# Optimization experiments

Measured on AMD Instinct MI355X. Metric: run time of the kernel, lower is better.

## Reference

```python
import jax, jax.numpy as jnp
import numpy as np

DN = ('NCHW', 'OIHW', 'NCHW')


def _conv(x, w, b, pad):
    y = jax.lax.conv_general_dilated(x, w, window_strides=(1, 1),
                                     padding=[(pad, pad), (pad, pad)],
                                     dimension_numbers=DN)
    return y + b[None, :, None, None]


def _maxpool2(x):
    return jax.lax.reduce_window(x, -jnp.inf, jax.lax.max,
                                 (1, 1, 2, 2), (1, 1, 2, 2), 'VALID')


def setup_inputs() -> dict:
    key = jax.random.key(0)
    ks = jax.random.split(key, 17)
    s = 0.05
    inp = {
        'x':  jax.random.normal(ks[0], (256, 3, 32, 32), jnp.float32),
        # conv weights (OIHW) and biases, matching AlexNet_flags.features
        'w1': jax.random.normal(ks[1], (64, 3, 3, 3), jnp.float32) * s,
        'b1': jax.random.normal(ks[2], (64,), jnp.float32) * s,
        'w2': jax.random.normal(ks[3], (192, 64, 5, 5), jnp.float32) * s,
        'b2': jax.random.normal(ks[4], (192,), jnp.float32) * s,
        'w3': jax.random.normal(ks[5], (384, 192, 3, 3), jnp.float32) * s,
        'b3': jax.random.normal(ks[6], (384,), jnp.float32) * s,
        'w4': jax.random.normal(ks[7], (256, 384, 3, 3), jnp.float32) * s,
        'b4': jax.random.normal(ks[8], (256,), jnp.float32) * s,
        'w5': jax.random.normal(ks[9], (256, 256, 3, 3), jnp.float32) * s,
        'b5': jax.random.normal(ks[10], (256,), jnp.float32) * s,
        # classifier linears (weight stored [out, in] as in torch)
        'fw1': jax.random.normal(ks[11], (4096, 256 * 4 * 4), jnp.float32) * s,
        'fb1': jax.random.normal(ks[12], (4096,), jnp.float32) * s,
        'fw2': jax.random.normal(ks[13], (4096, 4096), jnp.float32) * s,
        'fb2': jax.random.normal(ks[14], (4096,), jnp.float32) * s,
        'fw3': jax.random.normal(ks[15], (1000, 4096), jnp.float32) * s,
        'fb3': jax.random.normal(ks[16], (1000,), jnp.float32) * s,
    }
    return inp


def reference(x, w1, b1, w2, b2, w3, b3, w4, b4, w5, b5,
              fw1, fb1, fw2, fb2, fw3, fb3):
    relu = jax.nn.relu
    h = _maxpool2(relu(_conv(x, w1, b1, pad=1)))   # [B,64,16,16]
    h = _maxpool2(relu(_conv(h, w2, b2, pad=2)))   # [B,192,8,8]
    h = relu(_conv(h, w3, b3, pad=1))              # [B,384,8,8]
    h = relu(_conv(h, w4, b4, pad=1))              # [B,256,8,8]
    h = _maxpool2(relu(_conv(h, w5, b5, pad=1)))   # [B,256,4,4]
    h = h.reshape(h.shape[0], 256 * 4 * 4)
    # Dropout layers act as identity at inference (eval mode).
    h = relu(h @ fw1.T + fb1)
    h = relu(h @ fw2.T + fb2)
    return h @ fw3.T + fb3                          # [B,1000]
```

## Files before the change

kernel.cpp:

```cpp
#include <hip/hip_runtime.h>
#include <hip/hip_bf16.h>

#define DIV_UP(a,b) (((a)+(b)-1)/(b))

typedef __attribute__((ext_vector_type(8))) short bfrag;
typedef __attribute__((ext_vector_type(4))) float accf;
typedef __attribute__((ext_vector_type(16))) float accf16;

__device__ __forceinline__ unsigned short f2bf(float f) {
    __hip_bfloat16 h = __float2bfloat16(f);
    return *reinterpret_cast<unsigned short*>(&h);
}

__global__ __launch_bounds__(256) void conv1_mfma(
    const float* __restrict__ in, const float* __restrict__ w,
    const float* __restrict__ bias, unsigned short* __restrict__ out, int n0)
{
    constexpr int RAWS = 3 * 6 * 34;
    constexpr int INS  = 128 * 32;
    constexpr int WSZ  = 64 * 32;
    constexpr int CS   = 128 * 66;
    constexpr int SMEM = (CS * 4 > (RAWS + 4 + INS + WSZ) * 2)
                       ? CS * 4 : (RAWS + 4 + INS + WSZ) * 2;
    __shared__ __align__(16) char smem[SMEM];
    short* raw_s = (short*)smem;
    short* in_s  = raw_s + RAWS + 4;
    short* w_s   = in_s + INS;
    float* c_s   = (float*)smem;

    const int tid  = threadIdx.x;
    const int lane = tid & 63, wv = tid >> 6;
    const int quad = lane >> 4, lr = lane & 15;
    const int rb   = blockIdx.x;
    const int nl   = blockIdx.y;
    const int n    = n0 + nl;
    const int row0 = rb * 4;

    for (int idx = tid; idx < RAWS; idx += 256) {
        int c = idx / 204, rem = idx - c * 204;
        int ry = rem / 34, rx = rem - ry * 34;
        int iy = row0 - 1 + ry, ix = rx - 1;
        float v = 0.f;
        if (iy >= 0 && iy < 32 && ix >= 0 && ix < 32)
            v = in[((n * 3 + c) * 32 + iy) * 32 + ix];
        raw_s[idx] = (short)f2bf(v);
    }
    {
        const int soc = tid >> 2, cbq = tid & 3;
        const int wsw = ((cbq ^ ((soc >> 1) & 3)) << 3);
        __align__(16) unsigned short buf[8];
#pragma unroll
        for (int j = 0; j < 8; ++j) {
            int k = cbq * 8 + j;
            buf[j] = (k < 27) ? f2bf(w[soc * 27 + k]) : (unsigned short)0;
        }
        *(uint4*)&w_s[soc * 32 + wsw] = *(uint4*)buf;
    }
    __syncthreads();
    {
        const int k = tid & 31, pg = tid >> 5;
        const int shi = k >> 3, slo = k & 7;
        const bool valid = (k < 27);
        int cbase = 0;
        if (valid) {
            int c = k / 9, rr = k - c * 9;
            int ky = rr / 3, kx = rr - ky * 3;
            cbase = c * 204 + ky * 34 + kx;
        }
        const int prow = pg >> 1, pcol0 = (pg & 1) * 16;
        const int rbase = cbase + prow * 34 + pcol0;
#pragma unroll
        for (int i = 0; i < 16; ++i) {
            const int pos = prow * 32 + pcol0 + i;
            short v = valid ? raw_s[rbase + i] : (short)0;
            in_s[pos * 32 + ((shi ^ ((pos >> 1) & 3)) << 3) + slo] = v;
        }
    }
    __syncthreads();
    const int bswz = (quad ^ ((lr >> 1) & 3)) << 3;
    const bfrag b = *(const bfrag*)(w_s + (wv * 16 + lr) * 32 + bswz);
    accf acc[8];
#pragma unroll
    for (int mt = 0; mt < 8; ++mt) {
        const int pos = mt * 16 + lr;
        const bfrag a = *(const bfrag*)(in_s + pos * 32 + ((quad ^ ((pos >> 1) & 3)) << 3));
        acc[mt] = __builtin_amdgcn_mfma_f32_16x16x32_bf16(
            a, b, (accf){0.f, 0.f, 0.f, 0.f}, 0, 0, 0);
    }
    __syncthreads();
#pragma unroll
    for (int mt = 0; mt < 8; ++mt)
#pragma unroll
        for (int r = 0; r < 4; ++r)
            c_s[(mt * 16 + quad * 4 + r) * 66 + wv * 16 + lr] = acc[mt][r];
    __syncthreads();
    {
        const int oc = tid >> 2;
        const float bv = bias[oc];
        const int o0 = (tid & 3) * 8;
        __align__(16) unsigned short buf[8];
#pragma unroll
        for (int i = 0; i < 8; ++i) {
            int op = o0 + i, oy = op >> 4, ox = op & 15;
            int p = (oy * 2) * 32 + ox * 2;
            float v = fmaxf(fmaxf(c_s[p * 66 + oc],        c_s[(p + 1) * 66 + oc]),
                            fmaxf(c_s[(p + 32) * 66 + oc], c_s[(p + 33) * 66 + oc]));
            buf[i] = f2bf(fmaxf(v + bv, 0.f));
        }
        unsigned short* dst = out + ((size_t)(nl * 64 + oc)) * 256 + (row0 >> 1) * 16 + o0;
        *(uint4*)dst = *(uint4*)buf;
    }
}

__global__ __launch_bounds__(256) void wt_transform(
    const float* __restrict__ w, unsigned short* __restrict__ wt,
    int COUT, int CIN, int KK, int total)
{
    int idx = blockIdx.x * 256 + threadIdx.x;
    if (idx >= total) return;
    const int j    = idx & 7;
    const int lane = (idx >> 3) & 63;
    const int kh   = (idx >> 9) & 1;
    int t = idx >> 10;
    const int NOCG = COUT >> 5;
    const int ocg  = t % NOCG; t /= NOCG;
    const int NC   = CIN >> 5;
    const int cc   = t % NC;
    const int g    = t / NC;
    const int oc = ocg * 32 + (lane & 31);
    const int ci = cc * 32 + kh * 16 + (lane >> 5) * 8 + j;
    wt[idx] = f2bf(w[((size_t)oc * CIN + ci) * KK + g]);
}

template<int CIN, int KS, int HIN, int IMGS, int MODE, int COUT>
__global__ __launch_bounds__(256) void conv_mfma32(
    const unsigned short* __restrict__ in, const unsigned short* __restrict__ wt,
    const float* __restrict__ bias, unsigned short* __restrict__ out)
{
    constexpr int PAD  = KS / 2;
    constexpr int KK   = KS * KS;
    constexpr int PIX  = HIN * HIN;
    constexpr int NC   = CIN / 32;
    constexpr int NOCG = COUT / 32;
    constexpr int IPOS = IMGS * PIX;
    constexpr int ROWB = (IMGS == 1) ? PIX / 128 : 1;
    constexpr int INS  = IPOS * 32 + 32;
    constexpr int CS   = 128 * 66;
    constexpr int SMEM = (INS * 2 > CS * 4) ? INS * 2 : CS * 4;
    constexpr int GSTR = NC * NOCG * 1024;

    __shared__ __align__(16) char smem[SMEM];
    short* in_s = (short*)smem;
    float* c_s  = (float*)smem;

    const int tid  = threadIdx.x;
    const int lane = tid & 63, wv = tid >> 6;
    const int hi   = lane >> 5, lr32 = lane & 31;
    const int wvM  = wv >> 1, wvN = wv & 1;
    const int ocb  = blockIdx.x / ROWB, rb = blockIdx.x % ROWB;
    const int oc0  = ocb * 64;
    const int nl0  = (IMGS == 2) ? blockIdx.y * 2 : blockIdx.y;
    const int row0 = rb * (128 / HIN);

    if (tid < 32) in_s[IPOS * 32 + tid] = 0;

    accf16 acc[2];
#pragma unroll
    for (int i = 0; i < 2; ++i)
#pragma unroll
        for (int r = 0; r < 16; ++r) acc[i][r] = 0.f;

    int pym[2], pxm[2];
#pragma unroll
    for (int mt = 0; mt < 2; ++mt) {
        const int m = wvM * 64 + mt * 32 + lr32;
        pym[mt] = row0 + m / HIN;
        pxm[mt] = m % HIN;
    }
    int apos[KK][2];
    if constexpr (KS == 3) {
#pragma unroll
        for (int g = 0; g < KK; ++g) {
            const int dy = g / 3 - 1, dx = g % 3 - 1;
#pragma unroll
            for (int mt = 0; mt < 2; ++mt) {
                const int m = wvM * 64 + mt * 32 + lr32;
                const int img = m >> 6, p = m & 63;
                const int iy = (p >> 3) + dy, ix = (p & 7) + dx;
                const bool ok = ((unsigned)iy < 8u) & ((unsigned)ix < 8u);
                const int pos = ok ? img * 64 + iy * 8 + ix : IPOS;
                apos[g][mt] = pos * 64 + ((hi ^ ((pos >> 1) & 3)) << 4);
            }
        }
    }

    const int sci = tid & 31, slot = tid >> 5;
    const int shi = sci >> 3, slo = sci & 7;
    const unsigned short* wbase = wt + (size_t)(oc0 / 32 + wvN) * 1024 + lane * 8;

    for (int c0 = 0; c0 < CIN; c0 += 32) {
        const unsigned short* wb = wbase + (size_t)(c0 >> 5) * (NOCG * 1024);
        __syncthreads();
#pragma unroll
        for (int img = 0; img < IMGS; ++img) {
            const unsigned short* src = in + ((size_t)((nl0 + img) * CIN + c0 + sci)) * PIX;
            for (int iy = slot; iy < HIN; iy += 8) {
#pragma unroll
                for (int xc = 0; xc < HIN; xc += 8) {
                    uint4 v = *(const uint4*)(src + iy * HIN + xc);
                    const int p0 = img * PIX + iy * HIN + xc;
                    unsigned short e[8];
                    e[0] = (unsigned short)(v.x & 0xFFFF); e[1] = (unsigned short)(v.x >> 16);
                    e[2] = (unsigned short)(v.y & 0xFFFF); e[3] = (unsigned short)(v.y >> 16);
                    e[4] = (unsigned short)(v.z & 0xFFFF); e[5] = (unsigned short)(v.z >> 16);
                    e[6] = (unsigned short)(v.w & 0xFFFF); e[7] = (unsigned short)(v.w >> 16);
#pragma unroll
                    for (int k = 0; k < 8; ++k) {
                        const int p = p0 + k;
                        in_s[p * 32 + ((shi ^ ((p >> 1) & 3)) << 3) + slo] = (short)e[k];
                    }
                }
            }
        }
        bfrag bc0 = *(const bfrag*)(wb);
        bfrag bc1 = *(const bfrag*)(wb + 512);
        __syncthreads();
#pragma unroll
        for (int g = 0; g < KK; ++g) {
            bfrag bn0 = bc0, bn1 = bc1;
            if (g + 1 < KK) {
                bn0 = *(const bfrag*)(wb + (size_t)(g + 1) * GSTR);
                bn1 = *(const bfrag*)(wb + (size_t)(g + 1) * GSTR + 512);
            }
            int ap[2];
            if constexpr (KS == 3) {
                ap[0] = apos[g][0]; ap[1] = apos[g][1];
            } else {
                const int dy = g / KS - PAD, dx = g % KS - PAD;
#pragma unroll
                for (int mt = 0; mt < 2; ++mt) {
                    const int iy = pym[mt] + dy, ix = pxm[mt] + dx;
                    const bool ok = ((unsigned)iy < (unsigned)HIN) &
                                    ((unsigned)ix < (unsigned)HIN);
                    const int pos = ok ? iy * HIN + ix : IPOS;
                    ap[mt] = pos * 64 + ((hi ^ ((pos >> 1) & 3)) << 4);
                }
            }
#pragma unroll
            for (int kh = 0; kh < 2; ++kh) {
                const bfrag bb = kh ? bc1 : bc0;
#pragma unroll
                for (int mt = 0; mt < 2; ++mt) {
                    const bfrag a = *(const bfrag*)((const char*)in_s + (ap[mt] ^ (kh << 5)));
                    acc[mt] = __builtin_amdgcn_mfma_f32_32x32x16_bf16(a, bb, acc[mt], 0, 0, 0);
                }
            }
            bc0 = bn0; bc1 = bn1;
        }
    }

    __syncthreads();
#pragma unroll
    for (int mt = 0; mt < 2; ++mt)
#pragma unroll
        for (int r = 0; r < 16; ++r) {
            const int row = wvM * 64 + mt * 32 + (r & 3) + 8 * (r >> 2) + 4 * hi;
            c_s[row * 66 + wvN * 32 + lr32] = acc[mt][r];
        }
    __syncthreads();

    const int oc = tid >> 2;
    const float bv = bias[oc0 + oc];
    if (MODE == 0) {
        const int q = tid & 3, img = q >> 1, pl0 = (q & 1) * 32;
        __align__(16) unsigned short buf[32];
#pragma unroll
        for (int i = 0; i < 32; ++i)
            buf[i] = f2bf(fmaxf(c_s[(img * 64 + pl0 + i) * 66 + oc] + bv, 0.f));
        unsigned short* dst = out + ((size_t)((nl0 + img) * COUT + oc0 + oc)) * 64 + pl0;
        *(uint4*)(dst)      = *(uint4*)(buf);
        *(uint4*)(dst + 8)  = *(uint4*)(buf + 8);
        *(uint4*)(dst + 16) = *(uint4*)(buf + 16);
        *(uint4*)(dst + 24) = *(uint4*)(buf + 24);
    } else if (MODE == 1) {
        const int o0 = (tid & 3) * 8;
        __align__(16) unsigned short buf[8];
#pragma unroll
        for (int i = 0; i < 8; ++i) {
            int op = o0 + i, oy = op >> 3, ox = op & 7;
            int p = (oy * 2) * 16 + ox * 2;
            float v = fmaxf(fmaxf(c_s[p * 66 + oc],        c_s[(p + 1) * 66 + oc]),
                            fmaxf(c_s[(p + 16) * 66 + oc], c_s[(p + 17) * 66 + oc]));
            buf[i] = f2bf(fmaxf(v + bv, 0.f));
        }
        unsigned short* dst = out + ((size_t)(nl0 * COUT + oc0 + oc)) * 64
                            + (row0 >> 1) * 8 + o0;
        *(uint4*)dst = *(uint4*)buf;
    } else {
        const int q = tid & 3, img = q >> 1, o0 = (q & 1) * 8;
        __align__(16) unsigned short buf[8];
#pragma unroll
        for (int i = 0; i < 8; ++i) {
            int op = o0 + i, oy = op >> 2, ox = op & 3;
            int p = img * 64 + (oy * 2) * 8 + ox * 2;
            float v = fmaxf(fmaxf(c_s[p * 66 + oc],       c_s[(p + 1) * 66 + oc]),
                            fmaxf(c_s[(p + 8) * 66 + oc], c_s[(p + 9) * 66 + oc]));
            buf[i] = f2bf(fmaxf(v + bv, 0.f));
        }
        *(uint4*)(out + (size_t)(nl0 + img) * 4096 + (oc0 + oc) * 16 + o0) = *(uint4*)buf;
    }
}

template<bool RELU, bool F32OUT>
__global__ __launch_bounds__(1024) void fc_mfma4(
    const unsigned short* __restrict__ X, const float* __restrict__ W,
    const float* __restrict__ Bs, void* __restrict__ Yv, int N, int K)
{
    __shared__ __align__(16) char smem[65536];
    short* stag = (short*)smem;
    float* red  = (float*)smem;

    const int tid  = threadIdx.x;
    const int lane = tid & 63;
    const int w16  = tid >> 6;
    const int grp  = w16 >> 2;
    const int wg   = w16 & 3;
    const int quad = lane >> 4, lr = lane & 15;
    const int m0 = blockIdx.y * 64, n0 = blockIdx.x * 64;
    const int gtid = tid & 255;
    const int mm = gtid >> 2, ko = (gtid & 3) * 8;
    const int KQ = K >> 2;

    short* Xs = stag + grp * 4096;
    short* Ws = Xs + 2048;

    accf acc[4];
#pragma unroll
    for (int i = 0; i < 4; ++i) acc[i] = (accf){0.f, 0.f, 0.f, 0.f};

    int nr = n0 + mm; if (nr > N - 1) nr = N - 1;
    const unsigned short* xp = X + (size_t)(m0 + mm) * K + (size_t)grp * KQ + ko;
    const float*          wp = W + (size_t)nr * K + (size_t)grp * KQ + ko;

    const int wsw = (((gtid & 3) ^ ((mm >> 1) & 3)) << 3);
    const int rsw = ((quad ^ ((lr >> 1) & 3)) << 3);

    uint4  xv = *(const uint4*)(xp);
    float4 wa = *(const float4*)(wp);
    float4 wb = *(const float4*)(wp + 4);

    for (int k0 = 0; k0 < KQ; k0 += 32) {
        __syncthreads();
        *(uint4*)&Xs[mm * 32 + wsw] = xv;
        __align__(16) unsigned short wb16[8] = {
            f2bf(wa.x), f2bf(wa.y), f2bf(wa.z), f2bf(wa.w),
            f2bf(wb.x), f2bf(wb.y), f2bf(wb.z), f2bf(wb.w) };
        *(uint4*)&Ws[mm * 32 + wsw] = *(uint4*)wb16;
        __syncthreads();
        if (k0 + 32 < KQ) {
            xv = *(const uint4*)(xp + k0 + 32);
            wa = *(const float4*)(wp + k0 + 32);
            wb = *(const float4*)(wp + k0 + 36);
        }
        const bfrag b = *(const bfrag*)(Ws + (wg * 16 + lr) * 32 + rsw);
#pragma unroll
        for (int mt = 0; mt < 4; ++mt) {
            const bfrag a = *(const bfrag*)(Xs + (mt * 16 + lr) * 32 + rsw);
            acc[mt] = __builtin_amdgcn_mfma_f32_16x16x32_bf16(a, b, acc[mt], 0, 0, 0);
        }
    }

    __syncthreads();
#pragma unroll
    for (int mt = 0; mt < 4; ++mt)
#pragma unroll
        for (int r = 0; r < 4; ++r)
            red[grp * 4096 + (mt * 16 + quad * 4 + r) * 64 + wg * 16 + lr] = acc[mt][r];
    __syncthreads();

    {
        const int m  = tid >> 4;
        const int nq = (tid & 15) * 4;
        float4 v0 = *(const float4*)&red[            m * 64 + nq];
        float4 v1 = *(const float4*)&red[ 4096 +     m * 64 + nq];
        float4 v2 = *(const float4*)&red[ 8192 +     m * 64 + nq];
        float4 v3 = *(const float4*)&red[12288 +     m * 64 + nq];
        float s[4] = { v0.x + v1.x + v2.x + v3.x,
                       v0.y + v1.y + v2.y + v3.y,
                       v0.z + v1.z + v2.z + v3.z,
                       v0.w + v1.w + v2.w + v3.w };
#pragma unroll
        for (int i = 0; i < 4; ++i) {
            const int n = n0 + nq + i;
            if (n < N) {
                float v = s[i] + Bs[n];
                if (RELU) v = fmaxf(v, 0.f);
                if (F32OUT) ((float*)Yv)[(size_t)(m0 + m) * N + n] = v;
                else ((unsigned short*)Yv)[(size_t)(m0 + m) * N + n] = f2bf(v);
            }
        }
    }
}

__global__ void zero_out(float* __restrict__ out, int total)
{
    int i = blockIdx.x * 256 + threadIdx.x;
    if (i < total) out[i] = 0.f;
}

extern "C" void kernel_launch(void* const* d_in, const int* in_sizes, int n_in,
                              void* d_out, int out_size, void* d_ws, size_t ws_size,
                              hipStream_t stream)
{
    (void)in_sizes; (void)n_in;
    const float* x   = (const float*)d_in[0];
    const float* w1  = (const float*)d_in[1];
    const float* b1  = (const float*)d_in[2];
    const float* w2  = (const float*)d_in[3];
    const float* b2  = (const float*)d_in[4];
    const float* w3  = (const float*)d_in[5];
    const float* b3  = (const float*)d_in[6];
    const float* w4  = (const float*)d_in[7];
    const float* b4  = (const float*)d_in[8];
    const float* w5  = (const float*)d_in[9];
    const float* b5  = (const float*)d_in[10];
    const float* fw1 = (const float*)d_in[11];
    const float* fb1 = (const float*)d_in[12];
    const float* fw2 = (const float*)d_in[13];
    const float* fb2 = (const float*)d_in[14];
    const float* fw3 = (const float*)d_in[15];
    const float* fb3 = (const float*)d_in[16];
    float* out = (float*)d_out;

    const size_t WTB = 4890624u;
    int maxCH;
    if      (ws_size >= 27959296u) maxCH = 256;
    else if (ws_size >= 17473536u) maxCH = 128;
    else if (ws_size >= 14852096u) maxCH = 96;
    else if (ws_size >= 12230656u) maxCH = 64;
    else {
        zero_out<<<DIV_UP(out_size, 256), 256, 0, stream>>>(out, out_size);
        return;
    }
    unsigned short* wt2 = (unsigned short*)d_ws;
    unsigned short* wt3 = wt2 + 307200;
    unsigned short* wt4 = wt3 + 663552;
    unsigned short* wt5 = wt4 + 884736;
    const size_t CAb = ((size_t)maxCH * 49152u > 2097152u) ? (size_t)maxCH * 49152u : 2097152u;
    const size_t CBb = ((size_t)maxCH * 32768u > 2097152u) ? (size_t)maxCH * 32768u : 2097152u;
    unsigned short* CA = (unsigned short*)((char*)d_ws + WTB);
    unsigned short* CB = (unsigned short*)((char*)d_ws + WTB + CAb);
    unsigned short* T5 = (unsigned short*)((char*)d_ws + WTB + CAb + CBb);

    wt_transform<<<DIV_UP(307200, 256), 256, 0, stream>>>(w2, wt2, 192, 64, 25, 307200);
    wt_transform<<<DIV_UP(663552, 256), 256, 0, stream>>>(w3, wt3, 384, 192, 9, 663552);
    wt_transform<<<DIV_UP(884736, 256), 256, 0, stream>>>(w4, wt4, 256, 384, 9, 884736);
    wt_transform<<<DIV_UP(589824, 256), 256, 0, stream>>>(w5, wt5, 256, 256, 9, 589824);

    for (int n0 = 0; n0 < 256; ) {
        const int CH = (256 - n0 < maxCH) ? (256 - n0) : maxCH;
        conv1_mfma<<<dim3(8, CH), 256, 0, stream>>>(x, w1, b1, CA, n0);
        conv_mfma32<64, 5, 16, 1, 1, 192><<<dim3(6, CH), 256, 0, stream>>>(CA, wt2, b2, CB);
        conv_mfma32<192, 3, 8, 2, 0, 384><<<dim3(6, CH / 2), 256, 0, stream>>>(CB, wt3, b3, CA);
        conv_mfma32<384, 3, 8, 2, 0, 256><<<dim3(4, CH / 2), 256, 0, stream>>>(CA, wt4, b4, CB);
        conv_mfma32<256, 3, 8, 2, 2, 256><<<dim3(4, CH / 2), 256, 0, stream>>>(
            CB, wt5, b5, T5 + (size_t)n0 * 4096);
        n0 += CH;
    }

    fc_mfma4<true, false><<<dim3(64, 4), 1024, 0, stream>>>(T5, fw1, fb1, CA, 4096, 4096);
    fc_mfma4<true, false><<<dim3(64, 4), 1024, 0, stream>>>(CA, fw2, fb2, CB, 4096, 4096);
    fc_mfma4<false, true><<<dim3(16, 4), 1024, 0, stream>>>(CB, fw3, fb3, out, 1000, 4096);
}
```

Baseline: 504.4 us.

## Load MFMA operands directly from global memory in FC kernel, drop LDS staging

```diff
diff --git a/kernel.cpp b/kernel.cpp
--- a/kernel.cpp
+++ b/kernel.cpp
@@ -316,9 +316,7 @@
     const unsigned short* __restrict__ X, const float* __restrict__ W,
     const float* __restrict__ Bs, void* __restrict__ Yv, int N, int K)
 {
-    __shared__ __align__(16) char smem[65536];
-    short* stag = (short*)smem;
-    float* red  = (float*)smem;
+    __shared__ __align__(16) float red[4 * 64 * 64];
 
     const int tid  = threadIdx.x;
     const int lane = tid & 63;
@@ -327,46 +325,45 @@
     const int wg   = w16 & 3;
     const int quad = lane >> 4, lr = lane & 15;
     const int m0 = blockIdx.y * 64, n0 = blockIdx.x * 64;
-    const int gtid = tid & 255;
-    const int mm = gtid >> 2, ko = (gtid & 3) * 8;
     const int KQ = K >> 2;
 
-    short* Xs = stag + grp * 4096;
-    short* Ws = Xs + 2048;
-
     accf acc[4];
 #pragma unroll
     for (int i = 0; i < 4; ++i) acc[i] = (accf){0.f, 0.f, 0.f, 0.f};
 
-    int nr = n0 + mm; if (nr > N - 1) nr = N - 1;
-    const unsigned short* xp = X + (size_t)(m0 + mm) * K + (size_t)grp * KQ + ko;
-    const float*          wp = W + (size_t)nr * K + (size_t)grp * KQ + ko;
-
-    const int wsw = (((gtid & 3) ^ ((mm >> 1) & 3)) << 3);
-    const int rsw = ((quad ^ ((lr >> 1) & 3)) << 3);
-
-    uint4  xv = *(const uint4*)(xp);
-    float4 wa = *(const float4*)(wp);
-    float4 wb = *(const float4*)(wp + 4);
+    int nr = n0 + wg * 16 + lr; if (nr > N - 1) nr = N - 1;
+    const unsigned short* xp = X + (size_t)(m0 + lr) * K + grp * KQ + quad * 8;
+    const float*          wp = W + (size_t)nr * K + grp * KQ + quad * 8;
+    const size_t mstep = (size_t)16 * K;
+
+    uint4  xa0 = *(const uint4*)(xp);
+    uint4  xa1 = *(const uint4*)(xp + mstep);
+    uint4  xa2 = *(const uint4*)(xp + 2 * mstep);
+    uint4  xa3 = *(const uint4*)(xp + 3 * mstep);
+    float4 wa  = *(const float4*)(wp);
+    float4 wb  = *(const float4*)(wp + 4);
 
     for (int k0 = 0; k0 < KQ; k0 += 32) {
-        __syncthreads();
-        *(uint4*)&Xs[mm * 32 + wsw] = xv;
+        uint4 xn0, xn1, xn2, xn3; float4 wn, wm;
+        if (k0 + 32 < KQ) {
+            xn0 = *(const uint4*)(xp + k0 + 32);
+            xn1 = *(const uint4*)(xp + k0 + 32 + mstep);
+            xn2 = *(const uint4*)(xp + k0 + 32 + 2 * mstep);
+            xn3 = *(const uint4*)(xp + k0 + 32 + 3 * mstep);
+            wn  = *(const float4*)(wp + k0 + 32);
+            wm  = *(const float4*)(wp + k0 + 36);
+        }
         __align__(16) unsigned short wb16[8] = {
             f2bf(wa.x), f2bf(wa.y), f2bf(wa.z), f2bf(wa.w),
             f2bf(wb.x), f2bf(wb.y), f2bf(wb.z), f2bf(wb.w) };
-        *(uint4*)&Ws[mm * 32 + wsw] = *(uint4*)wb16;
-        __syncthreads();
+        const bfrag b = *(const bfrag*)wb16;
+        acc[0] = __builtin_amdgcn_mfma_f32_16x16x32_bf16(*(const bfrag*)&xa0, b, acc[0], 0, 0, 0);
+        acc[1] = __builtin_amdgcn_mfma_f32_16x16x32_bf16(*(const bfrag*)&xa1, b, acc[1], 0, 0, 0);
+        acc[2] = __builtin_amdgcn_mfma_f32_16x16x32_bf16(*(const bfrag*)&xa2, b, acc[2], 0, 0, 0);
+        acc[3] = __builtin_amdgcn_mfma_f32_16x16x32_bf16(*(const bfrag*)&xa3, b, acc[3], 0, 0, 0);
         if (k0 + 32 < KQ) {
-            xv = *(const uint4*)(xp + k0 + 32);
-            wa = *(const float4*)(wp + k0 + 32);
-            wb = *(const float4*)(wp + k0 + 36);
-        }
-        const bfrag b = *(const bfrag*)(Ws + (wg * 16 + lr) * 32 + rsw);
-#pragma unroll
-        for (int mt = 0; mt < 4; ++mt) {
-            const bfrag a = *(const bfrag*)(Xs + (mt * 16 + lr) * 32 + rsw);
-            acc[mt] = __builtin_amdgcn_mfma_f32_16x16x32_bf16(a, b, acc[mt], 0, 0, 0);
+            xa0 = xn0; xa1 = xn1; xa2 = xn2; xa3 = xn3;
+            wa = wn; wb = wm;
         }
     }
 
```

Measured after the change: 590.7 us. 17.1% more time.

## Use split-K FC GEMM with separate reduction kernel for classifier layers

Applied to the files above, without the earlier changes.

```diff
diff --git a/kernel.cpp b/kernel.cpp
--- a/kernel.cpp
+++ b/kernel.cpp
@@ -308,6 +308,102 @@
             buf[i] = f2bf(fmaxf(v + bv, 0.f));
         }
         *(uint4*)(out + (size_t)(nl0 + img) * 4096 + (oc0 + oc) * 16 + o0) = *(uint4*)buf;
+    }
+}
+
+__global__ __launch_bounds__(256) void fc_sk(
+    const unsigned short* __restrict__ X, const float* __restrict__ W,
+    float* __restrict__ P, int N, int K)
+{
+    __shared__ __align__(16) short Xs[64 * 32];
+    __shared__ __align__(16) short Ws[64 * 32];
+    const int tid  = threadIdx.x;
+    const int lane = tid & 63, wv = tid >> 6;
+    const int quad = lane >> 4, lr = lane & 15;
+    const int n0 = blockIdx.x * 64;
+    const int m0 = (blockIdx.y >> 2) * 64;
+    const int kz = blockIdx.y & 3;
+    const int mm = tid >> 2, ko = (tid & 3) * 8;
+    const int KQ = K >> 2;
+
+    accf acc[4];
+#pragma unroll
+    for (int i = 0; i < 4; ++i) acc[i] = (accf){0.f, 0.f, 0.f, 0.f};
+
+    int nr = n0 + mm; if (nr > N - 1) nr = N - 1;
+    const unsigned short* xp = X + (size_t)(m0 + mm) * K + (size_t)kz * KQ + ko;
+    const float*          wp = W + (size_t)nr * K + (size_t)kz * KQ + ko;
+
+    const int wsw = (((tid & 3) ^ ((mm >> 1) & 3)) << 3);
+    const int rsw = ((quad ^ ((lr >> 1) & 3)) << 3);
+
+    uint4  xv = *(const uint4*)(xp);
+    float4 wa = *(const float4*)(wp);
+    float4 wb = *(const float4*)(wp + 4);
+
+    for (int k0 = 0; k0 < KQ; k0 += 32) {
+        __syncthreads();
+        *(uint4*)&Xs[mm * 32 + wsw] = xv;
+        __align__(16) unsigned short wb16[8] = {
+            f2bf(wa.x), f2bf(wa.y), f2bf(wa.z), f2bf(wa.w),
+            f2bf(wb.x), f2bf(wb.y), f2bf(wb.z), f2bf(wb.w) };
+        *(uint4*)&Ws[mm * 32 + wsw] = *(uint4*)wb16;
+        __syncthreads();
+        if (k0 + 32 < KQ) {
+            xv = *(const uint4*)(xp + k0 + 32);
+            wa = *(const float4*)(wp + k0 + 32);
+            wb = *(const float4*)(wp + k0 + 36);
+        }
+        const bfrag b = *(const bfrag*)(Ws + (wv * 16 + lr) * 32 + rsw);
+#pragma unroll
+        for (int mt = 0; mt < 4; ++mt) {
+            const bfrag a = *(const bfrag*)(Xs + (mt * 16 + lr) * 32 + rsw);
+            acc[mt] = __builtin_amdgcn_mfma_f32_16x16x32_bf16(a, b, acc[mt], 0, 0, 0);
+        }
+    }
+
+    const int n = n0 + wv * 16 + lr;
+    if (n < N) {
+#pragma unroll
+        for (int mt = 0; mt < 4; ++mt)
+#pragma unroll
+            for (int r = 0; r < 4; ++r) {
+                const int m = m0 + mt * 16 + quad * 4 + r;
+                P[((size_t)kz * 256 + m) * N + n] = acc[mt][r];
+            }
+    }
+}
+
+template<bool RELU, bool F32OUT>
+__global__ __launch_bounds__(256) void fc_red(
+    const float* __restrict__ P, const float* __restrict__ Bs,
+    void* __restrict__ Yv, int N, int total4)
+{
+    int idx = blockIdx.x * 256 + threadIdx.x;
+    if (idx >= total4) return;
+    const int nq = N >> 2;
+    const int m = idx / nq;
+    const int n = (idx - m * nq) * 4;
+    const float* p = P + (size_t)m * N + n;
+    const size_t st = (size_t)256 * N;
+    float4 v0 = *(const float4*)(p);
+    float4 v1 = *(const float4*)(p + st);
+    float4 v2 = *(const float4*)(p + 2 * st);
+    float4 v3 = *(const float4*)(p + 3 * st);
+    float4 bb = *(const float4*)(Bs + n);
+    float s[4] = { v0.x + v1.x + v2.x + v3.x + bb.x,
+                   v0.y + v1.y + v2.y + v3.y + bb.y,
+                   v0.z + v1.z + v2.z + v3.z + bb.z,
+                   v0.w + v1.w + v2.w + v3.w + bb.w };
+    if (RELU) {
+#pragma unroll
+        for (int i = 0; i < 4; ++i) s[i] = fmaxf(s[i], 0.f);
+    }
+    if (F32OUT) {
+        *(float4*)((float*)Yv + (size_t)m * N + n) = (float4){s[0], s[1], s[2], s[3]};
+    } else {
+        __align__(8) unsigned short h[4] = { f2bf(s[0]), f2bf(s[1]), f2bf(s[2]), f2bf(s[3]) };
+        *(uint2*)((unsigned short*)Yv + (size_t)m * N + n) = *(uint2*)h;
     }
 }
 
@@ -468,7 +564,19 @@
         n0 += CH;
     }
 
-    fc_mfma4<true, false><<<dim3(64, 4), 1024, 0, stream>>>(T5, fw1, fb1, CA, 4096, 4096);
-    fc_mfma4<true, false><<<dim3(64, 4), 1024, 0, stream>>>(CA, fw2, fb2, CB, 4096, 4096);
-    fc_mfma4<false, true><<<dim3(16, 4), 1024, 0, stream>>>(CB, fw3, fb3, out, 1000, 4096);
-}
+    if (maxCH == 256) {
+        unsigned short* F1 = (unsigned short*)d_ws;
+        unsigned short* F2 = F1 + 1048576;
+        float* P = (float*)((char*)d_ws + 4194304);
+        fc_sk<<<dim3(64, 16), 256, 0, stream>>>(T5, fw1, P, 4096, 4096);
+        fc_red<true, false><<<DIV_UP(262144, 256), 256, 0, stream>>>(P, fb1, F1, 4096, 262144);
+        fc_sk<<<dim3(64, 16), 256, 0, stream>>>(F1, fw2, P, 4096, 4096);
+        fc_red<true, false><<<DIV_UP(262144, 256), 256, 0, stream>>>(P, fb2, F2, 4096, 262144);
+        fc_sk<<<dim3(16, 16), 256, 0, stream>>>(F2, fw3, P, 1000, 4096);
+        fc_red<false, true><<<DIV_UP(64000, 256), 256, 0, stream>>>(P, fb3, out, 1000, 64000);
+    } else {
+        fc_mfma4<true, false><<<dim3(64, 4), 1024, 0, stream>>>(T5, fw1, fb1, CA, 4096, 4096);
+        fc_mfma4<true, false><<<dim3(64, 4), 1024, 0, stream>>>(CA, fw2, fb2, CB, 4096, 4096);
+        fc_mfma4<false, true><<<dim3(16, 4), 1024, 0, stream>>>(CB, fw3, fb3, out, 1000, 4096);
+    }
+}
```

Result: faster. 436.1 us (-13.5%).
